# Performance work log

Hardware: AMD Instinct MI355X
Metric: run time of the kernel (lower is better)

## Reference

```python
import jax, jax.numpy as jnp
import numpy as np

N_ATOMS = 100_000
N_PAIRS = 3_200_000


def setup_inputs() -> dict:
    key = jax.random.key(0)
    k0, k1, k2, k3, k4 = jax.random.split(key, 5)
    atomic_numbers = jax.random.randint(k0, (N_ATOMS,), 1, 95, dtype=jnp.int32)
    distances = jax.random.uniform(k1, (N_PAIRS,), jnp.float32, 0.5, 5.0)
    cutoffs = jax.random.uniform(k2, (N_PAIRS,), jnp.float32)
    idx_i = jnp.sort(jax.random.randint(k3, (N_PAIRS,), 0, N_ATOMS, dtype=jnp.int32))
    idx_j = jax.random.randint(k4, (N_PAIRS,), 0, N_ATOMS, dtype=jnp.int32)
    # ZBL parameters (trainable=True defaults from __init__)
    a_coefficient = jnp.array([0.8854], dtype=jnp.float32)
    a_exponent = jnp.array([0.23], dtype=jnp.float32)
    phi_coefficients = jnp.array([0.18175, 0.50986, 0.28022, 0.02817], dtype=jnp.float32)
    phi_exponents = jnp.array([3.1998, 0.94229, 0.4029, 0.20162], dtype=jnp.float32)
    # unit conversion buffers: identity units -> factors = 1.0
    ke = jnp.array([1.0 / (4.0 * np.pi * 0.005526349406)], dtype=jnp.float32)
    distances_model2Ang = jnp.array([1.0], dtype=jnp.float32)
    energies_Hatree2model = jnp.array([1.0], dtype=jnp.float32)
    return dict(atomic_numbers=atomic_numbers, distances=distances, cutoffs=cutoffs,
                idx_i=idx_i, idx_j=idx_j, a_coefficient=a_coefficient,
                a_exponent=a_exponent, phi_coefficients=phi_coefficients,
                phi_exponents=phi_exponents, ke=ke,
                distances_model2Ang=distances_model2Ang,
                energies_Hatree2model=energies_Hatree2model)


def reference(atomic_numbers, distances, cutoffs, idx_i, idx_j,
              a_coefficient, a_exponent, phi_coefficients, phi_exponents,
              ke, distances_model2Ang, energies_Hatree2model):
    Z = atomic_numbers.astype(distances.dtype)            # [N]
    distances_ang = distances * distances_model2Ang        # [P]
    za = Z ** jnp.abs(a_exponent)                          # [N] (a_exponent is [1])
    a_ij = jnp.abs(a_coefficient) / (za[idx_i] + za[idx_j])  # [P]
    arguments = distances / a_ij                           # [P] (faithful: uses model-unit distances)
    # L1-normalized |phi_coefficients|
    abs_c = jnp.abs(phi_coefficients)
    coefficients = abs_c / jnp.sum(abs_c)                  # [4]
    exponents = jnp.abs(phi_exponents)                     # [4]
    # phi[p] = sum_k c_k * exp(-e_k * arg_p)  -> [P,4] intermediate
    phi = jnp.sum(coefficients[None, :] * jnp.exp(-exponents[None, :] * arguments[:, None]), axis=1)
    repulsion = ke * Z[idx_i] * Z[idx_j] / distances_ang * phi * cutoffs  # [P]
    Erep = energies_Hatree2model * jax.ops.segment_sum(repulsion, idx_i, num_segments=N_ATOMS)
    return Erep
```

## Files before the change

### kernel.cpp

```cpp
#include <hip/hip_runtime.h>
#include <math.h>

#define LOG2E 1.4426950408889634f

__global__ void __launch_bounds__(256)
zbl_prep(const int* __restrict__ Z, unsigned char* __restrict__ z8,
         float* __restrict__ out, int n_atoms, int out_n) {
    int i = blockIdx.x * blockDim.x + threadIdx.x;
    if (i < n_atoms) z8[i] = (unsigned char)Z[i];
    if (i < out_n)   out[i] = 0.0f;
}

__global__ void __launch_bounds__(256)
zbl_pairs4(const float* __restrict__ dist, const float* __restrict__ cut,
           const int* __restrict__ idx_i, const int* __restrict__ idx_j,
           const unsigned char* __restrict__ z8,
           const float* __restrict__ a_coef, const float* __restrict__ a_exp,
           const float* __restrict__ phi_c, const float* __restrict__ phi_e,
           const float* __restrict__ ke, const float* __restrict__ d2a,
           const float* __restrict__ e2m,
           float* __restrict__ out, int n) {
    __shared__ float za_tab[128];

    float aexp   = fabsf(a_exp[0]);
    float inv_ac = __fdividef(1.0f, fabsf(a_coef[0]));
    float c0 = fabsf(phi_c[0]), c1 = fabsf(phi_c[1]),
          c2 = fabsf(phi_c[2]), c3 = fabsf(phi_c[3]);
    float cnorm = __fdividef(1.0f, c0 + c1 + c2 + c3);
    c0 *= cnorm; c1 *= cnorm; c2 *= cnorm; c3 *= cnorm;
    float e0 = fabsf(phi_e[0]) * LOG2E, e1 = fabsf(phi_e[1]) * LOG2E,
          e2 = fabsf(phi_e[2]) * LOG2E, e3 = fabsf(phi_e[3]) * LOG2E;
    float scale = ke[0] * e2m[0] * __fdividef(1.0f, d2a[0]);

    int t = threadIdx.x;
    if (t < 128) za_tab[t] = (t >= 1) ? exp2f(aexp * __log2f((float)t)) : 0.0f;
    __syncthreads();

    int gid = blockIdx.x * blockDim.x + t;
    int p0 = gid * 4;

    int   k[4];
    float v[4];

    if (p0 + 3 < n) {
        float4 d4 = ((const float4*)dist)[gid];
        float4 c4 = ((const float4*)cut)[gid];
        int4   i4 = ((const int4*)idx_i)[gid];
        int4   j4 = ((const int4*)idx_j)[gid];
        k[0] = i4.x; k[1] = i4.y; k[2] = i4.z; k[3] = i4.w;

        int zi0 = (int)z8[i4.x], zi1 = (int)z8[i4.y],
            zi2 = (int)z8[i4.z], zi3 = (int)z8[i4.w];
        int zj0 = (int)z8[j4.x], zj1 = (int)z8[j4.y],
            zj2 = (int)z8[j4.z], zj3 = (int)z8[j4.w];

        float arg0 = d4.x * (za_tab[zi0] + za_tab[zj0]) * inv_ac;
        float arg1 = d4.y * (za_tab[zi1] + za_tab[zj1]) * inv_ac;
        float arg2 = d4.z * (za_tab[zi2] + za_tab[zj2]) * inv_ac;
        float arg3 = d4.w * (za_tab[zi3] + za_tab[zj3]) * inv_ac;

        float phi0 = c0 * exp2f(-e0 * arg0) + c1 * exp2f(-e1 * arg0)
                   + c2 * exp2f(-e2 * arg0) + c3 * exp2f(-e3 * arg0);
        float phi1 = c0 * exp2f(-e0 * arg1) + c1 * exp2f(-e1 * arg1)
                   + c2 * exp2f(-e2 * arg1) + c3 * exp2f(-e3 * arg1);
        float phi2 = c0 * exp2f(-e0 * arg2) + c1 * exp2f(-e1 * arg2)
                   + c2 * exp2f(-e2 * arg2) + c3 * exp2f(-e3 * arg2);
        float phi3 = c0 * exp2f(-e0 * arg3) + c1 * exp2f(-e1 * arg3)
                   + c2 * exp2f(-e2 * arg3) + c3 * exp2f(-e3 * arg3);

        v[0] = scale * (float)(zi0 * zj0) * phi0 * c4.x * __fdividef(1.0f, d4.x);
        v[1] = scale * (float)(zi1 * zj1) * phi1 * c4.y * __fdividef(1.0f, d4.y);
        v[2] = scale * (float)(zi2 * zj2) * phi2 * c4.z * __fdividef(1.0f, d4.z);
        v[3] = scale * (float)(zi3 * zj3) * phi3 * c4.w * __fdividef(1.0f, d4.w);
    } else {
        #pragma unroll
        for (int q = 0; q < 4; ++q) {
            int p = p0 + q;
            if (p < n) {
                int ki = idx_i[p], jj = idx_j[p];
                int zi = (int)z8[ki], zj = (int)z8[jj];
                float d = dist[p];
                float arg = d * (za_tab[zi] + za_tab[zj]) * inv_ac;
                float phi = c0 * exp2f(-e0 * arg) + c1 * exp2f(-e1 * arg)
                          + c2 * exp2f(-e2 * arg) + c3 * exp2f(-e3 * arg);
                k[q] = ki;
                v[q] = scale * (float)(zi * zj) * phi * cut[p] * __fdividef(1.0f, d);
            } else {
                k[q] = (q > 0) ? k[q - 1] : -1;
                v[q] = 0.0f;
            }
        }
    }

    float run = v[0];
    float firstRun = 0.0f;
    bool  firstEnds = false;
    int   runStart = 0;
    #pragma unroll
    for (int q = 1; q < 4; ++q) {
        if (k[q] == k[q - 1]) {
            run += v[q];
        } else {
            if (runStart == 0) { firstRun = run; firstEnds = true; }
            else if (k[q - 1] >= 0) atomicAdd(out + k[q - 1], run);
            run = v[q];
            runStart = q;
        }
    }
    float c   = run;
    int   key = k[3];

    int lane = t & 63;
    #pragma unroll
    for (int off = 1; off < 64; off <<= 1) {
        float ov = __shfl_up(c, (unsigned)off, 64);
        int   ok = __shfl_up(key, (unsigned)off, 64);
        if (lane >= off && ok == key) c += ov;
    }

    float prev_c   = __shfl_up(c, 1u, 64);
    int   prev_key = __shfl_up(key, 1u, 64);
    int   next_k0  = __shfl_down(k[0], 1u, 64);

    if (k[0] >= 0 && firstEnds) {
        float tot = firstRun + ((lane > 0 && prev_key == k[0]) ? prev_c : 0.0f);
        atomicAdd(out + k[0], tot);
    }
    bool tail = (lane == 63) || (next_k0 != key);
    if (key >= 0 && tail) atomicAdd(out + key, c);
}

extern "C" void kernel_launch(void* const* d_in, const int* in_sizes, int n_in,
                              void* d_out, int out_size, void* d_ws, size_t ws_size,
                              hipStream_t stream) {
    const int*   atomic_numbers = (const int*)  d_in[0];
    const float* distances      = (const float*)d_in[1];
    const float* cutoffs        = (const float*)d_in[2];
    const int*   idx_i          = (const int*)  d_in[3];
    const int*   idx_j          = (const int*)  d_in[4];
    const float* a_coefficient  = (const float*)d_in[5];
    const float* a_exponent     = (const float*)d_in[6];
    const float* phi_coeffs     = (const float*)d_in[7];
    const float* phi_exps       = (const float*)d_in[8];
    const float* ke             = (const float*)d_in[9];
    const float* d2a            = (const float*)d_in[10];
    const float* e2m            = (const float*)d_in[11];
    float* out = (float*)d_out;

    const int n_atoms = in_sizes[0];
    const int n_pairs = in_sizes[1];

    const int block = 256;
    const int n_threads = (n_pairs + 3) / 4;
    const int grid_pairs = (n_threads + block - 1) / block;
    const int grid_prep  = (((n_atoms > out_size) ? n_atoms : out_size) + block - 1) / block;

    unsigned char* z8 = (unsigned char*)d_ws;
    zbl_prep<<<grid_prep, block, 0, stream>>>(
        atomic_numbers, z8, out, n_atoms, out_size);
    zbl_pairs4<<<grid_pairs, block, 0, stream>>>(
        distances, cutoffs, idx_i, idx_j, z8,
        a_coefficient, a_exponent, phi_coeffs, phi_exps, ke, d2a, e2m,
        out, n_pairs);
}
```

Baseline: 118.5 us.

## Precompute per-atom Z^a table and process eight pairs per thread

```diff
diff --git a/kernel.cpp b/kernel.cpp
--- a/kernel.cpp
+++ b/kernel.cpp
@@ -4,25 +4,28 @@
 #define LOG2E 1.4426950408889634f
 
 __global__ void __launch_bounds__(256)
-zbl_prep(const int* __restrict__ Z, unsigned char* __restrict__ z8,
-         float* __restrict__ out, int n_atoms, int out_n) {
+zbl_prep(const int* __restrict__ Z, const float* __restrict__ a_exp,
+         float2* __restrict__ zaz, float* __restrict__ out,
+         int n_atoms, int out_n) {
     int i = blockIdx.x * blockDim.x + threadIdx.x;
-    if (i < n_atoms) z8[i] = (unsigned char)Z[i];
-    if (i < out_n)   out[i] = 0.0f;
+    float aexp = fabsf(a_exp[0]);
+    if (i < n_atoms) {
+        float zf = (float)Z[i];
+        float za = exp2f(aexp * __log2f(zf));
+        zaz[i] = make_float2(za, zf);
+    }
+    if (i < out_n) out[i] = 0.0f;
 }
 
 __global__ void __launch_bounds__(256)
-zbl_pairs4(const float* __restrict__ dist, const float* __restrict__ cut,
+zbl_pairs8(const float* __restrict__ dist, const float* __restrict__ cut,
            const int* __restrict__ idx_i, const int* __restrict__ idx_j,
-           const unsigned char* __restrict__ z8,
-           const float* __restrict__ a_coef, const float* __restrict__ a_exp,
+           const float2* __restrict__ zaz,
+           const float* __restrict__ a_coef,
            const float* __restrict__ phi_c, const float* __restrict__ phi_e,
            const float* __restrict__ ke, const float* __restrict__ d2a,
            const float* __restrict__ e2m,
            float* __restrict__ out, int n) {
-    __shared__ float za_tab[128];
-
-    float aexp   = fabsf(a_exp[0]);
     float inv_ac = __fdividef(1.0f, fabsf(a_coef[0]));
     float c0 = fabsf(phi_c[0]), c1 = fabsf(phi_c[1]),
           c2 = fabsf(phi_c[2]), c3 = fabsf(phi_c[3]);
@@ -32,59 +35,70 @@
           e2 = fabsf(phi_e[2]) * LOG2E, e3 = fabsf(phi_e[3]) * LOG2E;
     float scale = ke[0] * e2m[0] * __fdividef(1.0f, d2a[0]);
 
-    int t = threadIdx.x;
-    if (t < 128) za_tab[t] = (t >= 1) ? exp2f(aexp * __log2f((float)t)) : 0.0f;
-    __syncthreads();
+    int t   = threadIdx.x;
+    int gid = blockIdx.x * blockDim.x + t;
+    int p0  = gid * 8;
 
-    int gid = blockIdx.x * blockDim.x + t;
-    int p0 = gid * 4;
+    int   k[8];
+    float v[8];
 
-    int   k[4];
-    float v[4];
+    if (p0 + 7 < n) {
+        const float4* dist4 = (const float4*)dist;
+        const float4* cut4  = (const float4*)cut;
+        const int4*   ii4   = (const int4*)idx_i;
+        const int4*   jj4   = (const int4*)idx_j;
+        float4 dA = dist4[2 * gid], dB = dist4[2 * gid + 1];
+        float4 cA = cut4[2 * gid],  cB = cut4[2 * gid + 1];
+        int4   iA = ii4[2 * gid],   iB = ii4[2 * gid + 1];
+        int4   jA = jj4[2 * gid],   jB = jj4[2 * gid + 1];
 
-    if (p0 + 3 < n) {
-        float4 d4 = ((const float4*)dist)[gid];
-        float4 c4 = ((const float4*)cut)[gid];
-        int4   i4 = ((const int4*)idx_i)[gid];
-        int4   j4 = ((const int4*)idx_j)[gid];
-        k[0] = i4.x; k[1] = i4.y; k[2] = i4.z; k[3] = i4.w;
+        k[0] = iA.x; k[1] = iA.y; k[2] = iA.z; k[3] = iA.w;
+        k[4] = iB.x; k[5] = iB.y; k[6] = iB.z; k[7] = iB.w;
+        int j[8] = { jA.x, jA.y, jA.z, jA.w, jB.x, jB.y, jB.z, jB.w };
+        float d[8] = { dA.x, dA.y, dA.z, dA.w, dB.x, dB.y, dB.z, dB.w };
+        float cu[8] = { cA.x, cA.y, cA.z, cA.w, cB.x, cB.y, cB.z, cB.w };
 
-        int zi0 = (int)z8[i4.x], zi1 = (int)z8[i4.y],
-            zi2 = (int)z8[i4.z], zi3 = (int)z8[i4.w];
-        int zj0 = (int)z8[j4.x], zj1 = (int)z8[j4.y],
-            zj2 = (int)z8[j4.z], zj3 = (int)z8[j4.w];
+        float2 gj[8];
+        #pragma unroll
+        for (int q = 0; q < 8; ++q) gj[q] = zaz[j[q]];
 
-        float arg0 = d4.x * (za_tab[zi0] + za_tab[zj0]) * inv_ac;
-        float arg1 = d4.y * (za_tab[zi1] + za_tab[zj1]) * inv_ac;
-        float arg2 = d4.z * (za_tab[zi2] + za_tab[zj2]) * inv_ac;
-        float arg3 = d4.w * (za_tab[zi3] + za_tab[zj3]) * inv_ac;
+        float za_i[8], zf_i[8];
+        {
+            float2 g = zaz[k[0]];
+            za_i[0] = g.x; zf_i[0] = g.y;
+        }
+        #pragma unroll
+        for (int q = 1; q < 8; ++q) {
+            if (k[q] != k[q - 1]) {
+                float2 g = zaz[k[q]];
+                za_i[q] = g.x; zf_i[q] = g.y;
+            } else {
+                za_i[q] = za_i[q - 1]; zf_i[q] = zf_i[q - 1];
+            }
+        }
 
-        float phi0 = c0 * exp2f(-e0 * arg0) + c1 * exp2f(-e1 * arg0)
-                   + c2 * exp2f(-e2 * arg0) + c3 * exp2f(-e3 * arg0);
-        float phi1 = c0 * exp2f(-e0 * arg1) + c1 * exp2f(-e1 * arg1)
-                   + c2 * exp2f(-e2 * arg1) + c3 * exp2f(-e3 * arg1);
-        float phi2 = c0 * exp2f(-e0 * arg2) + c1 * exp2f(-e1 * arg2)
-                   + c2 * exp2f(-e2 * arg2) + c3 * exp2f(-e3 * arg2);
-        float phi3 = c0 * exp2f(-e0 * arg3) + c1 * exp2f(-e1 * arg3)
-                   + c2 * exp2f(-e2 * arg3) + c3 * exp2f(-e3 * arg3);
-
-        v[0] = scale * (float)(zi0 * zj0) * phi0 * c4.x * __fdividef(1.0f, d4.x);
-        v[1] = scale * (float)(zi1 * zj1) * phi1 * c4.y * __fdividef(1.0f, d4.y);
-        v[2] = scale * (float)(zi2 * zj2) * phi2 * c4.z * __fdividef(1.0f, d4.z);
-        v[3] = scale * (float)(zi3 * zj3) * phi3 * c4.w * __fdividef(1.0f, d4.w);
+        #pragma unroll
+        for (int q = 0; q < 8; ++q) {
+            float arg = d[q] * (za_i[q] + gj[q].x) * inv_ac;
+            float phi = c0 * exp2f(-e0 * arg) + c1 * exp2f(-e1 * arg)
+                      + c2 * exp2f(-e2 * arg) + c3 * exp2f(-e3 * arg);
+            v[q] = scale * zf_i[q] * gj[q].y * phi * cu[q]
+                 * __fdividef(1.0f, d[q]);
+        }
     } else {
         #pragma unroll
-        for (int q = 0; q < 4; ++q) {
+        for (int q = 0; q < 8; ++q) {
             int p = p0 + q;
             if (p < n) {
                 int ki = idx_i[p], jj = idx_j[p];
-                int zi = (int)z8[ki], zj = (int)z8[jj];
-                float d = dist[p];
-                float arg = d * (za_tab[zi] + za_tab[zj]) * inv_ac;
+                float2 gi = zaz[ki], gjv = zaz[jj];
+                float dd = dist[p];
+                float arg = dd * (gi.x + gjv.x) * inv_ac;
                 float phi = c0 * exp2f(-e0 * arg) + c1 * exp2f(-e1 * arg)
                           + c2 * exp2f(-e2 * arg) + c3 * exp2f(-e3 * arg);
                 k[q] = ki;
-                v[q] = scale * (float)(zi * zj) * phi * cut[p] * __fdividef(1.0f, d);
+                v[q] = scale * gi.y * gjv.y * phi * cut[p]
+                     * __fdividef(1.0f, dd);
             } else {
                 k[q] = (q > 0) ? k[q - 1] : -1;
                 v[q] = 0.0f;
@@ -97,7 +111,7 @@
     bool  firstEnds = false;
     int   runStart = 0;
     #pragma unroll
-    for (int q = 1; q < 4; ++q) {
+    for (int q = 1; q < 8; ++q) {
         if (k[q] == k[q - 1]) {
             run += v[q];
         } else {
@@ -108,7 +122,7 @@
         }
     }
     float c   = run;
-    int   key = k[3];
+    int   key = k[7];
 
     int lane = t & 63;
     #pragma unroll
@@ -151,15 +165,15 @@
     const int n_pairs = in_sizes[1];
 
     const int block = 256;
-    const int n_threads = (n_pairs + 3) / 4;
+    const int n_threads = (n_pairs + 7) / 8;
     const int grid_pairs = (n_threads + block - 1) / block;
     const int grid_prep  = (((n_atoms > out_size) ? n_atoms : out_size) + block - 1) / block;
 
-    unsigned char* z8 = (unsigned char*)d_ws;
+    float2* zaz = (float2*)d_ws;
     zbl_prep<<<grid_prep, block, 0, stream>>>(
-        atomic_numbers, z8, out, n_atoms, out_size);
-    zbl_pairs4<<<grid_pairs, block, 0, stream>>>(
-        distances, cutoffs, idx_i, idx_j, z8,
-        a_coefficient, a_exponent, phi_coeffs, phi_exps, ke, d2a, e2m,
+        atomic_numbers, a_exponent, zaz, out, n_atoms, out_size);
+    zbl_pairs8<<<grid_pairs, block, 0, stream>>>(
+        distances, cutoffs, idx_i, idx_j, zaz,
+        a_coefficient, phi_coeffs, phi_exps, ke, d2a, e2m,
         out, n_pairs);
 }
```

After: 123.7 us. 1.04x slower.
